# Performance work log

Hardware: AMD Instinct MI355X
Metric: run time of the kernel (lower is better)

## Reference

```python
import jax, jax.numpy as jnp
import numpy as np

B, TQ, TK = 2, 2048, 2048
D_IN, D_OUT, H = 1024, 1024, 16
HD = D_OUT // H  # head dim = 64


def setup_inputs() -> dict:
    key = jax.random.key(0)
    ks = jax.random.split(key, 11)
    s = 1.0 / np.sqrt(D_IN)
    so = 1.0 / np.sqrt(D_OUT)
    return {
        "q": jax.random.normal(ks[0], (B, TQ, D_IN), jnp.float32),
        "k": jax.random.normal(ks[1], (B, TK, D_IN), jnp.float32),
        "v": jax.random.normal(ks[2], (B, TK, D_IN), jnp.float32),
        "Wq": jax.random.uniform(ks[3], (D_OUT, D_IN), jnp.float32, -s, s),
        "bq": jax.random.uniform(ks[4], (D_OUT,), jnp.float32, -s, s),
        "Wk": jax.random.uniform(ks[5], (D_OUT, D_IN), jnp.float32, -s, s),
        "bk": jax.random.uniform(ks[6], (D_OUT,), jnp.float32, -s, s),
        "Wv": jax.random.uniform(ks[7], (D_OUT, D_IN), jnp.float32, -s, s),
        "bv": jax.random.uniform(ks[8], (D_OUT,), jnp.float32, -s, s),
        "Wo": jax.random.uniform(ks[9], (D_OUT, D_OUT), jnp.float32, -so, so),
        "bo": jax.random.uniform(ks[10], (D_OUT,), jnp.float32, -so, so),
    }


def reference(q, k, v, Wq, bq, Wk, bk, Wv, bv, Wo, bo):
    b, tq, _ = q.shape
    tk = k.shape[1]
    # linear projections, split heads: [B,T,D] -> [B,H,T,HD]
    qh = (q @ Wq.T + bq).reshape(b, tq, H, HD).transpose(0, 2, 1, 3)
    kh = (k @ Wk.T + bk).reshape(b, tk, H, HD).transpose(0, 2, 1, 3)
    vh = (v @ Wv.T + bv).reshape(b, tk, H, HD).transpose(0, 2, 1, 3)
    # scaled dot-product attention (forward never applies the causal mask)
    scores = jnp.einsum("bhqd,bhkd->bhqk", qh, kh) / np.sqrt(HD).astype(np.float32)
    attn = jax.nn.softmax(scores, axis=-1)
    x = jnp.einsum("bhqk,bhkd->bhqd", attn, vh)
    x = x.transpose(0, 2, 1, 3).reshape(b, tq, D_OUT)
    return x @ Wo.T + bo
```

## Files before the change

### kernel.cpp

```cpp
#include <hip/hip_runtime.h>
#include <hip/hip_bf16.h>

typedef __bf16 b16x8 __attribute__((ext_vector_type(8)));
typedef unsigned short u16x8 __attribute__((ext_vector_type(8)));
typedef unsigned short u16x4 __attribute__((ext_vector_type(4)));
typedef unsigned int u32x4 __attribute__((ext_vector_type(4)));
typedef unsigned int u32x2 __attribute__((ext_vector_type(2)));
typedef float f32x4 __attribute__((ext_vector_type(4)));
typedef float f32x16 __attribute__((ext_vector_type(16)));

__device__ __forceinline__ unsigned short f2b(float f) {
  unsigned u = __builtin_bit_cast(unsigned, f);
  u += 0x7fff + ((u >> 16) & 1);
  return (unsigned short)(u >> 16);
}

__device__ __forceinline__ b16x8 as_b(u16x8 v) { return __builtin_bit_cast(b16x8, v); }

__device__ __forceinline__ float fexp2(float x) {
#if __has_builtin(__builtin_amdgcn_exp2f)
  return __builtin_amdgcn_exp2f(x);
#else
  return exp2f(x);
#endif
}

__device__ __forceinline__ unsigned cvtpk(float lo, float hi) {
  unsigned r;
  asm("v_cvt_pk_bf16_f32 %0, %1, %2" : "=v"(r) : "v"(lo), "v"(hi));
  return r;
}

__device__ __forceinline__ void plswap(unsigned& a, unsigned& b) {
  asm volatile("v_permlane32_swap_b32 %0, %1" : "+v"(a), "+v"(b));
}

__device__ __forceinline__ b16x8 mkchunk(float p0, float p1, float p2, float p3,
                                         float p4, float p5, float p6, float p7) {
  unsigned a1 = cvtpk(p0, p1), b1 = cvtpk(p4, p5);
  unsigned a2 = cvtpk(p2, p3), b2 = cvtpk(p6, p7);
  plswap(a1, b1);
  plswap(a2, b2);
  u32x4 w = {a1, a2, b1, b2};
  return __builtin_bit_cast(b16x8, w);
}

#define AS1 __attribute__((address_space(1)))
#define AS3 __attribute__((address_space(3)))
__device__ __forceinline__ void gload_lds16(const void* g, void* l) {
  __builtin_amdgcn_global_load_lds((const AS1 void*)g, (AS3 void*)l, 16, 0, 0);
}

#define WAITV4() asm volatile("s_waitcnt vmcnt(4)" ::: "memory")
#define WAITV0() asm volatile("s_waitcnt vmcnt(0)" ::: "memory")
#define LGKM0()  asm volatile("s_waitcnt lgkmcnt(0)" ::: "memory")
#define BARRIER() asm volatile("s_barrier" ::: "memory")


__global__ __launch_bounds__(256) void convert_kernel(
    const float* __restrict__ q, const float* __restrict__ k, const float* __restrict__ v,
    const float* __restrict__ Wq, const float* __restrict__ Wk,
    const float* __restrict__ Wv, const float* __restrict__ Wo,
    unsigned short* __restrict__ qb, unsigned short* __restrict__ kb,
    unsigned short* __restrict__ vb, unsigned short* __restrict__ wqb,
    unsigned short* __restrict__ wkb, unsigned short* __restrict__ wvb,
    unsigned short* __restrict__ wob) {
  const float* src; unsigned short* dst; int rows;
  switch (blockIdx.y) {
    case 0: src = q;  dst = qb;  rows = 4096; break;
    case 1: src = k;  dst = kb;  rows = 4096; break;
    case 2: src = v;  dst = vb;  rows = 4096; break;
    case 3: src = Wq; dst = wqb; rows = 1024; break;
    case 4: src = Wk; dst = wkb; rows = 1024; break;
    case 5: src = Wv; dst = wvb; rows = 1024; break;
    default: src = Wo; dst = wob; rows = 1024; break;
  }
  const int row = blockIdx.x * 2 + (threadIdx.x >> 7);
  if (row >= rows) return;
  const int t = threadIdx.x & 127;
  const float* sp = src + (size_t)row * 1024 + t * 8;
  float4 f0 = *(const float4*)sp;
  float4 f1 = *(const float4*)(sp + 4);
  u16x8 h = { f2b(f0.x), f2b(f0.y), f2b(f0.z), f2b(f0.w),
              f2b(f1.x), f2b(f1.y), f2b(f1.z), f2b(f1.w) };
  const int swcol = ((t >> 3) << 6) | (((t & 7) ^ (row & 7)) << 3);
  *(u16x8*)(dst + (size_t)row * 1024 + swcol) = h;
}

template <int MODE, typename TOUT>
__device__ __forceinline__ void gemm_body(unsigned short* sA, unsigned short* sB,
                                          const unsigned short* __restrict__ A,
                                          const unsigned short* __restrict__ Bm,
                                          const float* __restrict__ bias,
                                          TOUT* __restrict__ C,
                                          int bm, int bn) {
  const int tid = threadIdx.x;
  const int l = tid & 63, w = tid >> 6;
  const int wm = w >> 1, wn = w & 1;
  const int lr = l & 15, lg = l >> 4;
  const int r8 = l >> 3, sl = l & 7;

  f32x4 acc[2][4] = {};

  for (int k0 = 0; k0 < 1024; k0 += 64) {
#pragma unroll
    for (int i = 0; i < 2; ++i) {
      const int row = i * 32 + w * 8 + r8;
      gload_lds16(A + (size_t)(bm + row) * 1024 + k0 + sl * 8, &sA[i * 2048 + w * 512]);
    }
#pragma unroll
    for (int i = 0; i < 4; ++i) {
      const int row = i * 32 + w * 8 + r8;
      gload_lds16(Bm + (size_t)(bn + row) * 1024 + k0 + sl * 8, &sB[i * 2048 + w * 512]);
    }
    __syncthreads();

    b16x8 af[2][2], bf[4][2];
#pragma unroll
    for (int mb = 0; mb < 2; ++mb)
#pragma unroll
      for (int kh = 0; kh < 2; ++kh) {
        const int r = wm * 32 + mb * 16 + lr;
        af[mb][kh] = as_b(*(const u16x8*)(&sA[(r * 64 + kh * 32 + lg * 8) ^ ((r & 7) << 3)]));
      }
#pragma unroll
    for (int nb = 0; nb < 4; ++nb)
#pragma unroll
      for (int kh = 0; kh < 2; ++kh) {
        const int r = wn * 64 + nb * 16 + lr;
        bf[nb][kh] = as_b(*(const u16x8*)(&sB[(r * 64 + kh * 32 + lg * 8) ^ ((r & 7) << 3)]));
      }
#pragma unroll
    for (int mb = 0; mb < 2; ++mb)
#pragma unroll
      for (int nb = 0; nb < 4; ++nb) {
        acc[mb][nb] = __builtin_amdgcn_mfma_f32_16x16x32_bf16(af[mb][0], bf[nb][0], acc[mb][nb], 0, 0, 0);
        acc[mb][nb] = __builtin_amdgcn_mfma_f32_16x16x32_bf16(af[mb][1], bf[nb][1], acc[mb][nb], 0, 0, 0);
      }
    __syncthreads();
  }

  const float qscale = 0.125f * 1.44269504f;
#pragma unroll
  for (int mb = 0; mb < 2; ++mb)
#pragma unroll
    for (int nb = 0; nb < 4; ++nb) {
      const int c = bn + wn * 64 + nb * 16 + lr;
      const float bv = bias[c];
      const int r0 = bm + wm * 32 + mb * 16 + lg * 4;
      if constexpr (MODE == 2) {
        const int hh = c >> 6, hd = c & 63;
        const int bb = r0 >> 11, t0 = r0 & 2047;
        u16x4 pk = { f2b(acc[mb][nb][0] + bv), f2b(acc[mb][nb][1] + bv),
                     f2b(acc[mb][nb][2] + bv), f2b(acc[mb][nb][3] + bv) };
        const int tsw = (t0 & ~63) | (((((t0 >> 3) & 7) ^ (hd & 7)) << 3)) | (t0 & 7);
        *(u16x4*)(&C[(((size_t)bb * 16 + hh) * 64 + hd) * 2048 + tsw]) = pk;
      } else {
#pragma unroll
        for (int i = 0; i < 4; ++i) {
          float val = acc[mb][nb][i] + bv;
          if constexpr (MODE == 1) val *= qscale;
          if constexpr (MODE == 3) {
            C[(size_t)(r0 + i) * 1024 + c] = val;
          } else {
            const int cc = (c & ~63) | (((((c >> 3) & 7) ^ ((r0 + i) & 7)) << 3)) | (c & 7);
            C[(size_t)(r0 + i) * 1024 + cc] = (TOUT)f2b(val);
          }
        }
      }
    }
}

__global__ __launch_bounds__(256) void proj_kernel(
    const unsigned short* __restrict__ qb, const unsigned short* __restrict__ kb,
    const unsigned short* __restrict__ vb,
    const unsigned short* __restrict__ wqb, const float* __restrict__ bq,
    const unsigned short* __restrict__ wkb, const float* __restrict__ bk,
    const unsigned short* __restrict__ wvb, const float* __restrict__ bv,
    unsigned short* __restrict__ Qh, unsigned short* __restrict__ Kh,
    unsigned short* __restrict__ Vt) {
  __shared__ __align__(16) unsigned short sA[64 * 64];
  __shared__ __align__(16) unsigned short sB[128 * 64];
  const int id = blockIdx.x;
  const int bn = (id / 192) * 128;
  const int w_ = id % 192;
  const int bz = w_ / 64;
  const int bm = (w_ % 64) * 64;
  if (bz == 0)      gemm_body<1, unsigned short>(sA, sB, qb, wqb, bq, Qh, bm, bn);
  else if (bz == 1) gemm_body<0, unsigned short>(sA, sB, kb, wkb, bk, Kh, bm, bn);
  else              gemm_body<2, unsigned short>(sA, sB, vb, wvb, bv, Vt, bm, bn);
}

__global__ __launch_bounds__(256) void out_kernel(
    const unsigned short* __restrict__ X, const unsigned short* __restrict__ wob,
    const float* __restrict__ bo, float* __restrict__ out) {
  __shared__ __align__(16) unsigned short sA[64 * 64];
  __shared__ __align__(16) unsigned short sB[128 * 64];
  const int id = blockIdx.x;
  const int bn = (id / 64) * 128;
  const int bm = (id % 64) * 64;
  gemm_body<3, float>(sA, sB, X, wob, bo, out, bm, bn);
}

__global__ __launch_bounds__(512, 4) void attn_kernel(
    const unsigned short* __restrict__ Qh, const unsigned short* __restrict__ Kh,
    const unsigned short* __restrict__ Vt, unsigned short* __restrict__ X) {
  __shared__ __align__(16) unsigned short sMem[8][4096];

  const int tid = threadIdx.x;
  const int l = tid & 63, wq = tid >> 6;
  const int half = wq >> 2, w4 = wq & 3;
  const int lq = l & 31, lg = l >> 5;

  const int id = blockIdx.x + (int)(gridDim.x * blockIdx.y);
  const int id2 = (id & 7) * 64 + (id >> 3);
  const int bx = id2 & 15, by = id2 >> 4;
  const int b = by >> 4, h = by & 15;
  const int q0 = bx * 128 + w4 * 32;
  const int kvbase = half * 1024;

  const size_t baseQK = (size_t)b * 2048 * 1024 + (size_t)h * 64;
  const size_t baseV  = ((size_t)(b * 16 + h)) * 64 * 2048;

  unsigned short* sK0 = &sMem[half * 4 + 0][0];
  unsigned short* sK1 = &sMem[half * 4 + 1][0];
  unsigned short* sV0 = &sMem[half * 4 + 2][0];
  unsigned short* sV1 = &sMem[half * 4 + 3][0];

  const int rk = lq & 7;
  b16x8 qf0, qf1, qf2, qf3;
  {
    const unsigned short* qp = Qh + baseQK + (size_t)(q0 + lq) * 1024;
    qf0 = as_b(*(const u16x8*)(qp + (((0 + lg) ^ rk) << 3)));
    qf1 = as_b(*(const u16x8*)(qp + (((2 + lg) ^ rk) << 3)));
    qf2 = as_b(*(const u16x8*)(qp + (((4 + lg) ^ rk) << 3)));
    qf3 = as_b(*(const u16x8*)(qp + (((6 + lg) ^ rk) << 3)));
  }

  const int r8 = l >> 3, sl = l & 7;

  auto stageKV = [&](unsigned short* dK, unsigned short* dV, int kv0) {
#pragma unroll
    for (int i = 0; i < 2; ++i) {
      const int rowb = 16 * w4 + 8 * i;
      gload_lds16(Kh + baseQK + (size_t)(kv0 + rowb + r8) * 1024 + sl * 8, dK + rowb * 64);
      gload_lds16(Vt + baseV + (size_t)(rowb + r8) * 2048 + kv0 + sl * 8, dV + rowb * 64);
    }
  };

  float m_run = 0.f, l_run = 0.f;
  f32x16 Oa = {}, Ob = {};
  const int sw = (lq & 7) << 3;

  auto body = [&](const unsigned short* K_, const unsigned short* V_) {
    f32x16 s0, s1;
#pragma unroll
    for (int j = 0; j < 16; ++j) { s0[j] = -m_run; s1[j] = -m_run; }
    __builtin_amdgcn_s_setprio(1);
#pragma unroll
    for (int c = 0; c < 4; ++c) {
      const int hd8 = c * 16 + 8 * lg;
      b16x8 kf0 = as_b(*(const u16x8*)(&K_[lq * 64 + (hd8 ^ sw)]));
      b16x8 kf1 = as_b(*(const u16x8*)(&K_[(32 + lq) * 64 + (hd8 ^ sw)]));
      b16x8 qf = (c == 0) ? qf0 : (c == 1) ? qf1 : (c == 2) ? qf2 : qf3;
      s0 = __builtin_amdgcn_mfma_f32_32x32x16_bf16(kf0, qf, s0, 0, 0, 0);
      s1 = __builtin_amdgcn_mfma_f32_32x32x16_bf16(kf1, qf, s1, 0, 0, 0);
    }
    __builtin_amdgcn_s_setprio(0);

    float a0 = fmaxf(fmaxf(s0[0], s0[1]), fmaxf(s0[2], s0[3]));
    float a1 = fmaxf(fmaxf(s0[4], s0[5]), fmaxf(s0[6], s0[7]));
    float a2 = fmaxf(fmaxf(s0[8], s0[9]), fmaxf(s0[10], s0[11]));
    float a3 = fmaxf(fmaxf(s0[12], s0[13]), fmaxf(s0[14], s0[15]));
    float a4 = fmaxf(fmaxf(s1[0], s1[1]), fmaxf(s1[2], s1[3]));
    float a5 = fmaxf(fmaxf(s1[4], s1[5]), fmaxf(s1[6], s1[7]));
    float a6 = fmaxf(fmaxf(s1[8], s1[9]), fmaxf(s1[10], s1[11]));
    float a7 = fmaxf(fmaxf(s1[12], s1[13]), fmaxf(s1[14], s1[15]));
    float mx = fmaxf(fmaxf(fmaxf(a0, a1), fmaxf(a2, a3)),
                     fmaxf(fmaxf(a4, a5), fmaxf(a6, a7)));
    mx = fmaxf(mx, __shfl_xor(mx, 32));

    if (__any(mx > 8.0f)) {
      const float dm = fmaxf(mx, 0.f);
      const float al = fexp2(-dm);
      m_run += dm;
      l_run *= al;
#pragma unroll
      for (int j = 0; j < 16; ++j) {
        Oa[j] *= al; Ob[j] *= al; s0[j] -= dm; s1[j] -= dm;
      }
    }

#pragma unroll
    for (int j = 0; j < 16; ++j) s0[j] = fexp2(s0[j]);
#pragma unroll
    for (int j = 0; j < 16; ++j) s1[j] = fexp2(s1[j]);

    float r0 = ((s0[0] + s0[1]) + (s0[2] + s0[3])) + ((s0[4] + s0[5]) + (s0[6] + s0[7]));
    float r1 = ((s0[8] + s0[9]) + (s0[10] + s0[11])) + ((s0[12] + s0[13]) + (s0[14] + s0[15]));
    float r2 = ((s1[0] + s1[1]) + (s1[2] + s1[3])) + ((s1[4] + s1[5]) + (s1[6] + s1[7]));
    float r3 = ((s1[8] + s1[9]) + (s1[10] + s1[11])) + ((s1[12] + s1[13]) + (s1[14] + s1[15]));
    float rs = (r0 + r1) + (r2 + r3);
    rs += __shfl_xor(rs, 32);
    l_run += rs;

    b16x8 pb0 = mkchunk(s0[0], s0[1], s0[2], s0[3], s0[4], s0[5], s0[6], s0[7]);
    b16x8 pb1 = mkchunk(s0[8], s0[9], s0[10], s0[11], s0[12], s0[13], s0[14], s0[15]);
    b16x8 pb2 = mkchunk(s1[0], s1[1], s1[2], s1[3], s1[4], s1[5], s1[6], s1[7]);
    b16x8 pb3 = mkchunk(s1[8], s1[9], s1[10], s1[11], s1[12], s1[13], s1[14], s1[15]);

    __builtin_amdgcn_s_setprio(1);
#pragma unroll
    for (int c = 0; c < 4; ++c) {
      const int kv8 = c * 16 + 8 * lg;
      b16x8 vfa = as_b(*(const u16x8*)(&V_[lq * 64 + (kv8 ^ sw)]));
      b16x8 vfb = as_b(*(const u16x8*)(&V_[(32 + lq) * 64 + (kv8 ^ sw)]));
      b16x8 pb = (c == 0) ? pb0 : (c == 1) ? pb1 : (c == 2) ? pb2 : pb3;
      Oa = __builtin_amdgcn_mfma_f32_32x32x16_bf16(vfa, pb, Oa, 0, 0, 0);
      Ob = __builtin_amdgcn_mfma_f32_32x32x16_bf16(vfb, pb, Ob, 0, 0, 0);
    }
    __builtin_amdgcn_s_setprio(0);
  };

  stageKV(sK0, sV0, kvbase);
  stageKV(sK1, sV1, kvbase + 64);

#pragma unroll 1
  for (int tt = 0; tt < 16; tt += 2) {
    WAITV4();
    BARRIER();
    body(sK0, sV0);
    LGKM0();
    BARRIER();
    if (tt + 2 < 16) stageKV(sK0, sV0, kvbase + (tt + 2) * 64);

    if (tt + 3 < 16) { WAITV4(); } else { WAITV0(); }
    BARRIER();
    body(sK1, sV1);
    LGKM0();
    BARRIER();
    if (tt + 3 < 16) stageKV(sK1, sV1, kvbase + (tt + 3) * 64);
  }

  float* fb = (float*)&sMem[0][0];
  const int mbase = w4 * 64 + l;
  if (half == 1) {
    fb[0 * 256 + mbase] = m_run;
    fb[1 * 256 + mbase] = l_run;
#pragma unroll
    for (int j = 0; j < 16; ++j) fb[(2 + j) * 256 + mbase] = Oa[j];
#pragma unroll
    for (int j = 0; j < 16; ++j) fb[(18 + j) * 256 + mbase] = Ob[j];
  }
  __syncthreads();
  if (half == 0) {
    const float m2 = fb[0 * 256 + mbase], l2 = fb[1 * 256 + mbase];
    const float mM = fmaxf(m_run, m2);
    const float c1 = fexp2(m_run - mM), c2 = fexp2(m2 - mM);
    const float inv = 1.0f / (l_run * c1 + l2 * c2);
    const float ia = c1 * inv, ib = c2 * inv;
#pragma unroll
    for (int j = 0; j < 16; ++j) {
      Oa[j] = Oa[j] * ia + fb[(2 + j) * 256 + mbase] * ib;
      Ob[j] = Ob[j] * ia + fb[(18 + j) * 256 + mbase] * ib;
    }
    unsigned short* xp = X + baseQK + (size_t)(q0 + lq) * 1024;
#pragma unroll
    for (int g = 0; g < 4; ++g) {
      u32x2 wa = { cvtpk(Oa[4 * g + 0], Oa[4 * g + 1]),
                   cvtpk(Oa[4 * g + 2], Oa[4 * g + 3]) };
      *(u32x2*)(xp + ((g ^ rk) << 3) + 4 * lg) = wa;
      u32x2 wb = { cvtpk(Ob[4 * g + 0], Ob[4 * g + 1]),
                   cvtpk(Ob[4 * g + 2], Ob[4 * g + 3]) };
      *(u32x2*)(xp + (((4 + g) ^ rk) << 3) + 4 * lg) = wb;
    }
  }
}

extern "C" void kernel_launch(void* const* d_in, const int* in_sizes, int n_in,
                              void* d_out, int out_size, void* d_ws, size_t ws_size,
                              hipStream_t stream) {
  const float* q  = (const float*)d_in[0];
  const float* k  = (const float*)d_in[1];
  const float* v  = (const float*)d_in[2];
  const float* Wq = (const float*)d_in[3];
  const float* bq = (const float*)d_in[4];
  const float* Wk = (const float*)d_in[5];
  const float* bk = (const float*)d_in[6];
  const float* Wv = (const float*)d_in[7];
  const float* bv = (const float*)d_in[8];
  const float* Wo = (const float*)d_in[9];
  const float* bo = (const float*)d_in[10];

  unsigned short* ws = (unsigned short*)d_ws;
  const size_t M1 = (size_t)1024 * 1024;
  unsigned short* qb  = ws;
  unsigned short* kb  = ws + 4 * M1;
  unsigned short* vb  = ws + 8 * M1;
  unsigned short* wqb = ws + 12 * M1;
  unsigned short* wkb = ws + 13 * M1;
  unsigned short* wvb = ws + 14 * M1;
  unsigned short* wob = ws + 15 * M1;
  unsigned short* Qh  = ws + 16 * M1;
  unsigned short* Kh  = ws + 20 * M1;
  unsigned short* Vt  = ws + 24 * M1;
  unsigned short* X   = qb;

  dim3 blk(256);
  convert_kernel<<<dim3(2048, 7), blk, 0, stream>>>(q, k, v, Wq, Wk, Wv, Wo,
                                                    qb, kb, vb, wqb, wkb, wvb, wob);
  proj_kernel<<<dim3(1536), blk, 0, stream>>>(qb, kb, vb, wqb, bq, wkb, bk, wvb, bv,
                                              Qh, Kh, Vt);
  attn_kernel<<<dim3(16, 32), dim3(512), 0, stream>>>(Qh, Kh, Vt, X);
  out_kernel<<<dim3(512), blk, 0, stream>>>(X, wob, bo, (float*)d_out);
}
```

Before: 117.5 us.

## Fuse fp32-to-bf16 activation conversion into projection GEMM A-tile loads

The separate conversion pass over q, k, v is removed. The projection GEMM now reads fp32 activations directly, converts them to bf16 in registers and writes swizzled tiles to LDS; only the weights are still pre-converted. This drops one full write and re-read of the 24 MB bf16 activation copies. In exchange the A-tile path loses asynchronous global-to-LDS loads, and because each activation tile is reused by 8 column blocks, the fp32 reads and conversion are repeated for each of them.

```diff
diff --git a/kernel.cpp b/kernel.cpp
--- a/kernel.cpp
+++ b/kernel.cpp
@@ -58,25 +58,18 @@
 
 
 __global__ __launch_bounds__(256) void convert_kernel(
-    const float* __restrict__ q, const float* __restrict__ k, const float* __restrict__ v,
     const float* __restrict__ Wq, const float* __restrict__ Wk,
     const float* __restrict__ Wv, const float* __restrict__ Wo,
-    unsigned short* __restrict__ qb, unsigned short* __restrict__ kb,
-    unsigned short* __restrict__ vb, unsigned short* __restrict__ wqb,
-    unsigned short* __restrict__ wkb, unsigned short* __restrict__ wvb,
-    unsigned short* __restrict__ wob) {
-  const float* src; unsigned short* dst; int rows;
+    unsigned short* __restrict__ wqb, unsigned short* __restrict__ wkb,
+    unsigned short* __restrict__ wvb, unsigned short* __restrict__ wob) {
+  const float* src; unsigned short* dst;
   switch (blockIdx.y) {
-    case 0: src = q;  dst = qb;  rows = 4096; break;
-    case 1: src = k;  dst = kb;  rows = 4096; break;
-    case 2: src = v;  dst = vb;  rows = 4096; break;
-    case 3: src = Wq; dst = wqb; rows = 1024; break;
-    case 4: src = Wk; dst = wkb; rows = 1024; break;
-    case 5: src = Wv; dst = wvb; rows = 1024; break;
-    default: src = Wo; dst = wob; rows = 1024; break;
+    case 0: src = Wq; dst = wqb; break;
+    case 1: src = Wk; dst = wkb; break;
+    case 2: src = Wv; dst = wvb; break;
+    default: src = Wo; dst = wob; break;
   }
   const int row = blockIdx.x * 2 + (threadIdx.x >> 7);
-  if (row >= rows) return;
   const int t = threadIdx.x & 127;
   const float* sp = src + (size_t)row * 1024 + t * 8;
   float4 f0 = *(const float4*)sp;
@@ -87,9 +80,9 @@
   *(u16x8*)(dst + (size_t)row * 1024 + swcol) = h;
 }
 
-template <int MODE, typename TOUT>
+template <int MODE, int AFP32, typename TOUT>
 __device__ __forceinline__ void gemm_body(unsigned short* sA, unsigned short* sB,
-                                          const unsigned short* __restrict__ A,
+                                          const void* __restrict__ Av,
                                           const unsigned short* __restrict__ Bm,
                                           const float* __restrict__ bias,
                                           TOUT* __restrict__ C,
@@ -103,10 +96,25 @@
   f32x4 acc[2][4] = {};
 
   for (int k0 = 0; k0 < 1024; k0 += 64) {
-#pragma unroll
-    for (int i = 0; i < 2; ++i) {
-      const int row = i * 32 + w * 8 + r8;
-      gload_lds16(A + (size_t)(bm + row) * 1024 + k0 + sl * 8, &sA[i * 2048 + w * 512]);
+    if constexpr (AFP32) {
+      const int arow = tid >> 2, aseg = (tid & 3) * 16;
+      const float* ap = (const float*)Av + (size_t)(bm + arow) * 1024 + k0 + aseg;
+      float4 f0 = *(const float4*)(ap);
+      float4 f1 = *(const float4*)(ap + 4);
+      float4 f2 = *(const float4*)(ap + 8);
+      float4 f3 = *(const float4*)(ap + 12);
+      u32x4 h0 = { cvtpk(f0.x, f0.y), cvtpk(f0.z, f0.w),
+                   cvtpk(f1.x, f1.y), cvtpk(f1.z, f1.w) };
+      u32x4 h1 = { cvtpk(f2.x, f2.y), cvtpk(f2.z, f2.w),
+                   cvtpk(f3.x, f3.y), cvtpk(f3.z, f3.w) };
+      *(u32x4*)(&sA[(arow * 64 + aseg) ^ ((arow & 7) << 3)]) = h0;
+      *(u32x4*)(&sA[(arow * 64 + aseg + 8) ^ ((arow & 7) << 3)]) = h1;
+    } else {
+#pragma unroll
+      for (int i = 0; i < 2; ++i) {
+        gload_lds16((const unsigned short*)Av + (size_t)(bm + i * 32 + w * 8 + r8) * 1024 + k0 + sl * 8,
+                    &sA[i * 2048 + w * 512]);
+      }
     }
 #pragma unroll
     for (int i = 0; i < 4; ++i) {
@@ -172,8 +180,7 @@
 }
 
 __global__ __launch_bounds__(256) void proj_kernel(
-    const unsigned short* __restrict__ qb, const unsigned short* __restrict__ kb,
-    const unsigned short* __restrict__ vb,
+    const float* __restrict__ q, const float* __restrict__ k, const float* __restrict__ v,
     const unsigned short* __restrict__ wqb, const float* __restrict__ bq,
     const unsigned short* __restrict__ wkb, const float* __restrict__ bk,
     const unsigned short* __restrict__ wvb, const float* __restrict__ bv,
@@ -186,9 +193,9 @@
   const int w_ = id % 192;
   const int bz = w_ / 64;
   const int bm = (w_ % 64) * 64;
-  if (bz == 0)      gemm_body<1, unsigned short>(sA, sB, qb, wqb, bq, Qh, bm, bn);
-  else if (bz == 1) gemm_body<0, unsigned short>(sA, sB, kb, wkb, bk, Kh, bm, bn);
-  else              gemm_body<2, unsigned short>(sA, sB, vb, wvb, bv, Vt, bm, bn);
+  if (bz == 0)      gemm_body<1, 1, unsigned short>(sA, sB, q, wqb, bq, Qh, bm, bn);
+  else if (bz == 1) gemm_body<0, 1, unsigned short>(sA, sB, k, wkb, bk, Kh, bm, bn);
+  else              gemm_body<2, 1, unsigned short>(sA, sB, v, wvb, bv, Vt, bm, bn);
 }
 
 __global__ __launch_bounds__(256) void out_kernel(
@@ -199,7 +206,7 @@
   const int id = blockIdx.x;
   const int bn = (id / 64) * 128;
   const int bm = (id % 64) * 64;
-  gemm_body<3, float>(sA, sB, X, wob, bo, out, bm, bn);
+  gemm_body<3, 0, float>(sA, sB, X, wob, bo, out, bm, bn);
 }
 
 __global__ __launch_bounds__(512, 4) void attn_kernel(
@@ -394,9 +401,6 @@
 
   unsigned short* ws = (unsigned short*)d_ws;
   const size_t M1 = (size_t)1024 * 1024;
-  unsigned short* qb  = ws;
-  unsigned short* kb  = ws + 4 * M1;
-  unsigned short* vb  = ws + 8 * M1;
   unsigned short* wqb = ws + 12 * M1;
   unsigned short* wkb = ws + 13 * M1;
   unsigned short* wvb = ws + 14 * M1;
@@ -404,12 +408,11 @@
   unsigned short* Qh  = ws + 16 * M1;
   unsigned short* Kh  = ws + 20 * M1;
   unsigned short* Vt  = ws + 24 * M1;
-  unsigned short* X   = qb;
+  unsigned short* X   = ws;
 
   dim3 blk(256);
-  convert_kernel<<<dim3(2048, 7), blk, 0, stream>>>(q, k, v, Wq, Wk, Wv, Wo,
-                                                    qb, kb, vb, wqb, wkb, wvb, wob);
-  proj_kernel<<<dim3(1536), blk, 0, stream>>>(qb, kb, vb, wqb, bq, wkb, bk, wvb, bv,
+  convert_kernel<<<dim3(512, 4), blk, 0, stream>>>(Wq, Wk, Wv, Wo, wqb, wkb, wvb, wob);
+  proj_kernel<<<dim3(1536), blk, 0, stream>>>(q, k, v, wqb, bq, wkb, bk, wvb, bv,
                                               Qh, Kh, Vt);
   attn_kernel<<<dim3(16, 32), dim3(512), 0, stream>>>(Qh, Kh, Vt, X);
   out_kernel<<<dim3(512), blk, 0, stream>>>(X, wob, bo, (float*)d_out);
```

Result: slower. 125.5 us (+6.8%).
